# Optimization experiments

Hardware: AMD Instinct MI355X
Metric: run time of the kernel (lower is better)

Reference implementation:

```python
import jax, jax.numpy as jnp
import numpy as np

NUM_HEADS = 16


def setup_inputs() -> dict:
    key = jax.random.key(0)
    k1, k2, k3 = jax.random.split(key, 3)
    B, S, D = 2, 2048, 1024
    x = jax.random.normal(k1, (B, S, D), dtype=jnp.float32)
    # qkv_bias=False -> no bias on qkv projection; output Dense has default bias
    w_qkv = jax.random.normal(k2, (D, 3 * D), dtype=jnp.float32) * (1.0 / np.sqrt(D))
    w_out = jax.random.normal(k3, (D, D), dtype=jnp.float32) * (1.0 / np.sqrt(D))
    b_out = jnp.zeros((D,), dtype=jnp.float32)
    return {"x": x, "w_qkv": w_qkv, "w_out": w_out, "b_out": b_out}


def reference(x, w_qkv, w_out, b_out):
    B, S, D = x.shape
    H = NUM_HEADS
    Dh = D // H
    scale = 1.0 / np.sqrt(Dh).astype(np.float32)

    qkv = jnp.einsum('bsd,de->bse', x, w_qkv)           # [B,S,3D]
    q, k, v = jnp.split(qkv, 3, axis=-1)
    split = lambda t: t.reshape(B, S, H, Dh).transpose(0, 2, 1, 3)  # [B,H,S,Dh]
    q, k, v = split(q), split(k), split(v)

    attn = jnp.einsum('bhid,bhjd->bhij', q, k) * scale  # [B,H,S,S]
    # mask=None -> all-ones mask combined with causal mask => causal float mask
    causal = jnp.tril(jnp.ones((S, S), dtype=jnp.float32))[None, None]
    attn = causal * attn + (1.0 - causal) * (-1e9)
    attn = jax.nn.softmax(attn, axis=-1)

    out = jnp.einsum('bhij,bhjd->bhid', attn, v)        # [B,H,S,Dh]
    out = out.transpose(0, 2, 1, 3).reshape(B, S, D)    # merge heads
    return jnp.einsum('bsd,de->bse', out, w_out) + b_out
```

## Files before the change

kernel.cpp:

```cpp
#include <hip/hip_runtime.h>

typedef unsigned short u16;
typedef __bf16 bf16x8 __attribute__((ext_vector_type(8)));
typedef unsigned short u16x8 __attribute__((ext_vector_type(8)));
typedef float f32x4 __attribute__((ext_vector_type(4)));

union Frag { u16x8 u; bf16x8 b; };

__device__ __forceinline__ u16 f2bf(float f) {
  unsigned u = __builtin_bit_cast(unsigned, f);
  u += 0x7fff + ((u >> 16) & 1);
  return (u16)(u >> 16);
}

__device__ __forceinline__ f32x4 mfma16(bf16x8 a, bf16x8 b, f32x4 c) {
  return __builtin_amdgcn_mfma_f32_16x16x32_bf16(a, b, c, 0, 0, 0);
}

typedef const __attribute__((address_space(1))) void* as1cv;
typedef __attribute__((address_space(3))) void* as3v;

__device__ __forceinline__ void glds16(const u16* g, u16* l) {
  __builtin_amdgcn_global_load_lds((as1cv)g, (as3v)l, 16, 0, 0);
}

__global__ __launch_bounds__(256) void castf_bf(const float* __restrict__ src,
                                                u16* __restrict__ dst, int n4) {
  int i = blockIdx.x * blockDim.x + threadIdx.x;
  int stride = gridDim.x * blockDim.x;
  for (; i < n4; i += stride) {
    float4 v = ((const float4*)src)[i];
    ushort4 o;
    o.x = f2bf(v.x); o.y = f2bf(v.y); o.z = f2bf(v.z); o.w = f2bf(v.w);
    ((ushort4*)dst)[i] = o;
  }
}

__global__ __launch_bounds__(256) void cast_transpose(const float* __restrict__ src,
                                                      u16* __restrict__ dst, int K, int N) {
  __shared__ float tile[32][33];
  int tn = N >> 5;
  int bk = blockIdx.x / tn, bn = blockIdx.x % tn;
  int k0 = bk << 5, n0 = bn << 5;
  int tx = threadIdx.x, ty = threadIdx.y;
#pragma unroll
  for (int i = 0; i < 4; i++)
    tile[ty + 8 * i][tx] = src[(size_t)(k0 + ty + 8 * i) * N + n0 + tx];
  __syncthreads();
#pragma unroll
  for (int i = 0; i < 4; i++)
    dst[(size_t)(n0 + ty + 8 * i) * K + k0 + tx] = f2bf(tile[tx][ty + 8 * i]);
}

template <int FP32OUT>
__global__ __launch_bounds__(256) void gemm_bt(const u16* __restrict__ A,
                                               const u16* __restrict__ BT,
                                               void* __restrict__ Cout,
                                               const float* __restrict__ bias,
                                               int N, int K, int nbc) {
  __shared__ u16 Al[128 * 32];
  __shared__ u16 Bl[128 * 32];
  int bid = blockIdx.x;
  int br = bid / nbc, bc = bid % nbc;
  int tid = threadIdx.x;
  int w = tid >> 6, l = tid & 63;
  int lg = l >> 4, lq = l & 15;
  int wr = w >> 1, wc = w & 1;

  f32x4 acc[4][4];
#pragma unroll
  for (int m = 0; m < 4; m++)
#pragma unroll
    for (int n = 0; n < 4; n++)
      acc[m][n] = (f32x4){0.f, 0.f, 0.f, 0.f};

  const u16* Ab = A + (size_t)(br * 128 + 32 * w + (l >> 2)) * K + (l & 3) * 8;
  const u16* Bb = BT + (size_t)(bc * 128 + 32 * w + (l >> 2)) * K + (l & 3) * 8;
  u16* Ald = Al + 32 * w * 32;
  u16* Bld = Bl + 32 * w * 32;

  for (int kt = 0; kt < K; kt += 32) {
    glds16(Ab + kt, Ald);
    glds16(Ab + (size_t)16 * K + kt, Ald + 16 * 32);
    glds16(Bb + kt, Bld);
    glds16(Bb + (size_t)16 * K + kt, Bld + 16 * 32);
    __syncthreads();

    Frag af[4], bf[4];
#pragma unroll
    for (int m = 0; m < 4; m++)
      af[m].u = *(const u16x8*)(Al + (64 * wr + 16 * m + lq) * 32 + lg * 8);
#pragma unroll
    for (int n = 0; n < 4; n++)
      bf[n].u = *(const u16x8*)(Bl + (64 * wc + 16 * n + lq) * 32 + lg * 8);
#pragma unroll
    for (int m = 0; m < 4; m++)
#pragma unroll
      for (int n = 0; n < 4; n++)
        acc[m][n] = mfma16(af[m].b, bf[n].b, acc[m][n]);
    __syncthreads();
  }

  int row0 = br * 128 + 64 * wr + lg * 4;
  int col0 = bc * 128 + 64 * wc + lq;
  if (FP32OUT) {
    float* C = (float*)Cout;
#pragma unroll
    for (int n = 0; n < 4; n++) {
      float bv = bias[col0 + 16 * n];
#pragma unroll
      for (int m = 0; m < 4; m++)
#pragma unroll
        for (int r = 0; r < 4; r++)
          C[(size_t)(row0 + 16 * m + r) * N + col0 + 16 * n] = acc[m][n][r] + bv;
    }
  } else {
    u16* C = (u16*)Cout;
#pragma unroll
    for (int n = 0; n < 4; n++)
#pragma unroll
      for (int m = 0; m < 4; m++)
#pragma unroll
        for (int r = 0; r < 4; r++)
          C[(size_t)(row0 + 16 * m + r) * N + col0 + 16 * n] = f2bf(acc[m][n][r]);
  }
}

__global__ __launch_bounds__(256) void build_vt(const u16* __restrict__ qkv,
                                                u16* __restrict__ vt) {
  __shared__ u16 t[64][65];
  int bid = blockIdx.x;
  int s0 = (bid & 31) * 64;
  int bh = bid >> 5;
  int b = bh >> 4, h = bh & 15;
  int tid = threadIdx.x;
  int r = tid >> 2, c4 = (tid & 3) * 16;
  const u16* srow = qkv + (size_t)(b * 2048 + s0 + r) * 3072 + 2048 + h * 64 + c4;
  u16x8 v0 = *(const u16x8*)(srow);
  u16x8 v1 = *(const u16x8*)(srow + 8);
#pragma unroll
  for (int j = 0; j < 8; j++) { t[r][c4 + j] = v0[j]; t[r][c4 + 8 + j] = v1[j]; }
  __syncthreads();
  int dh = tid >> 2, sc = (tid & 3) * 16;
  u16 outv[16];
#pragma unroll
  for (int i = 0; i < 16; ++i) {
    int e = sc + i;
    int b32 = e >> 5, e32 = e & 31;
    int k = ((e32 >> 2) & 1) * 16 + (e32 >> 3) * 4 + (e32 & 3);
    outv[i] = t[b32 * 32 + k][dh];
  }
  u16* drow = vt + ((size_t)bh * 64 + dh) * 2048 + s0 + sc;
  *(u16x8*)drow = *(u16x8*)&outv[0];
  *(u16x8*)(drow + 8) = *(u16x8*)&outv[8];
}

__global__ __launch_bounds__(256) void flash_attn(const u16* __restrict__ qkv,
                                                  const u16* __restrict__ vt,
                                                  u16* __restrict__ aout) {
  __shared__ __align__(16) u16 pool[2][8192];
  const float SCALE = 0.125f;
  int bid = blockIdx.x;
  int qb = 31 - (bid >> 5);
  int bh = bid & 31;
  int b = bh >> 4, h = bh & 15;
  int tid = threadIdx.x;
  int w = tid >> 6, l = tid & 63;
  int lg = l >> 4, lq = l & 15;
  int q0w = qb * 64 + w * 16;
  int qidx = q0w + lq;

  const size_t rs = 3072;
  Frag qf0, qf1;
  const u16* qbase = qkv + (size_t)(b * 2048 + q0w + lq) * rs + h * 64 + lg * 8;
  qf0.u = *(const u16x8*)(qbase);
  qf1.u = *(const u16x8*)(qbase + 32);

  int srw = l >> 3;
  int scol = 8 * ((l & 7) ^ srw);
  const u16* kg = qkv + (size_t)(b * 2048) * rs + 1024 + h * 64;
  const u16* vg = vt + (size_t)bh * 64 * 2048;
  int r0 = (w * 2 + 0) * 8 + srw;
  int r1 = (w * 2 + 1) * 8 + srw;

  float m = -1e38f, lam = 0.f;
  f32x4 o[4];
#pragma unroll
  for (int d = 0; d < 4; ++d) o[d] = (f32x4){0.f, 0.f, 0.f, 0.f};
  int ntiles = qb + 1;

  glds16(kg + (size_t)r0 * rs + scol, &pool[0][(w * 2 + 0) * 512]);
  glds16(kg + (size_t)r1 * rs + scol, &pool[0][(w * 2 + 1) * 512]);
  glds16(vg + (size_t)r0 * 2048 + scol, &pool[0][4096 + (w * 2 + 0) * 512]);
  glds16(vg + (size_t)r1 * 2048 + scol, &pool[0][4096 + (w * 2 + 1) * 512]);
  __syncthreads();

  int swz = (lq & 7) << 3;
  for (int t = 0; t < ntiles; ++t) {
    int cur = t & 1;
    if (t + 1 < ntiles) {
      int kt2 = (t + 1) * 64;
      u16* nb = &pool[cur ^ 1][0];
      glds16(kg + (size_t)(kt2 + r0) * rs + scol, nb + (w * 2 + 0) * 512);
      glds16(kg + (size_t)(kt2 + r1) * rs + scol, nb + (w * 2 + 1) * 512);
      glds16(vg + (size_t)r0 * 2048 + kt2 + scol, nb + 4096 + (w * 2 + 0) * 512);
      glds16(vg + (size_t)r1 * 2048 + kt2 + scol, nb + 4096 + (w * 2 + 1) * 512);
    }
    int kt = t * 64;
    const u16* Kl = &pool[cur][0];
    const u16* Vl = &pool[cur][4096];

    f32x4 s[4];
#pragma unroll
    for (int sub = 0; sub < 4; ++sub) {
      int row = sub * 16 + lq;
      Frag k0, k1;
      k0.u = *(const u16x8*)(Kl + row * 64 + ((lg * 8) ^ swz));
      k1.u = *(const u16x8*)(Kl + row * 64 + ((32 + lg * 8) ^ swz));
      f32x4 z = {0.f, 0.f, 0.f, 0.f};
      s[sub] = mfma16(k0.b, qf0.b, z);
      s[sub] = mfma16(k1.b, qf1.b, s[sub]);
    }

    float tm = -1e38f;
    float sv[4][4];
    if (t == qb) {
#pragma unroll
      for (int sub = 0; sub < 4; ++sub)
#pragma unroll
        for (int r = 0; r < 4; ++r) {
          int key = kt + sub * 16 + lg * 4 + r;
          float v = s[sub][r] * SCALE;
          if (key > qidx) v = -1e30f;
          sv[sub][r] = v;
          tm = fmaxf(tm, v);
        }
    } else {
#pragma unroll
      for (int sub = 0; sub < 4; ++sub)
#pragma unroll
        for (int r = 0; r < 4; ++r) {
          float v = s[sub][r] * SCALE;
          sv[sub][r] = v;
          tm = fmaxf(tm, v);
        }
    }
    tm = fmaxf(tm, __shfl_xor(tm, 16));
    tm = fmaxf(tm, __shfl_xor(tm, 32));
    float mn = fmaxf(m, tm);
    float alpha = __expf(m - mn);
    float psum = 0.f;
    unsigned pp[4][2];
#pragma unroll
    for (int sub = 0; sub < 4; ++sub) {
#pragma unroll
      for (int tt = 0; tt < 2; ++tt) {
        float p0 = __expf(sv[sub][2 * tt] - mn);
        float p1 = __expf(sv[sub][2 * tt + 1] - mn);
        psum += p0 + p1;
        pp[sub][tt] = (unsigned)f2bf(p0) | ((unsigned)f2bf(p1) << 16);
      }
    }
    psum += __shfl_xor(psum, 16);
    psum += __shfl_xor(psum, 32);
    lam = lam * alpha + psum;
    m = mn;
#pragma unroll
    for (int d = 0; d < 4; ++d)
#pragma unroll
      for (int r = 0; r < 4; ++r) o[d][r] *= alpha;

#pragma unroll
    for (int hf = 0; hf < 2; ++hf) {
      union { unsigned w4[4]; u16x8 u; bf16x8 bv; } pf;
      pf.w4[0] = pp[2 * hf][0];
      pf.w4[1] = pp[2 * hf][1];
      pf.w4[2] = pp[2 * hf + 1][0];
      pf.w4[3] = pp[2 * hf + 1][1];
#pragma unroll
      for (int d = 0; d < 4; ++d) {
        int row = d * 16 + lq;
        Frag vf;
        vf.u = *(const u16x8*)(Vl + row * 64 + ((hf * 32 + lg * 8) ^ swz));
        o[d] = mfma16(vf.b, pf.bv, o[d]);
      }
    }
    __syncthreads();
  }

  float inv = 1.0f / lam;
  u16* Ost = &pool[0][0] + w * (16 * 72);
#pragma unroll
  for (int d = 0; d < 4; ++d)
#pragma unroll
    for (int r = 0; r < 4; ++r)
      Ost[lq * 72 + d * 16 + lg * 4 + r] = f2bf(o[d][r] * inv);
  int q = l >> 2, c16 = (l & 3) * 16;
  u16x8 t0, t1;
#pragma unroll
  for (int j = 0; j < 8; j++) { t0[j] = Ost[q * 72 + c16 + j]; t1[j] = Ost[q * 72 + c16 + 8 + j]; }
  u16* orow = aout + (size_t)(b * 2048 + qb * 64 + w * 16 + q) * 1024 + h * 64 + c16;
  *(u16x8*)orow = t0;
  *(u16x8*)(orow + 8) = t1;
}

extern "C" void kernel_launch(void* const* d_in, const int* in_sizes, int n_in,
                              void* d_out, int out_size, void* d_ws, size_t ws_size,
                              hipStream_t stream) {
  const float* x    = (const float*)d_in[0];
  const float* wqkv = (const float*)d_in[1];
  const float* wout = (const float*)d_in[2];
  const float* bout = (const float*)d_in[3];
  float* out = (float*)d_out;

  char* ws = (char*)d_ws;
  u16* xb    = (u16*)(ws);
  u16* wqkvT = (u16*)(ws + 8388608);
  u16* woutT = (u16*)(ws + 14680064);
  u16* qkvb  = (u16*)(ws + 16777216);
  u16* vtb   = (u16*)(ws + 41943040);
  u16* aoutb = (u16*)(ws + 50331648);

  castf_bf<<<1024, 256, 0, stream>>>(x, xb, (4096 * 1024) / 4);
  cast_transpose<<<(1024 / 32) * (3072 / 32), dim3(32, 8), 0, stream>>>(wqkv, wqkvT, 1024, 3072);
  cast_transpose<<<(1024 / 32) * (1024 / 32), dim3(32, 8), 0, stream>>>(wout, woutT, 1024, 1024);

  gemm_bt<0><<<(4096 / 128) * (3072 / 128), 256, 0, stream>>>(xb, wqkvT, qkvb, nullptr,
                                                              3072, 1024, 3072 / 128);
  build_vt<<<1024, 256, 0, stream>>>(qkvb, vtb);
  flash_attn<<<2 * 16 * (2048 / 64), 256, 0, stream>>>(qkvb, vtb, aoutb);

  gemm_bt<1><<<(4096 / 128) * (1024 / 128), 256, 0, stream>>>(aoutb, woutT, out, bout,
                                                              1024, 1024, 1024 / 128);
}
```

Baseline: 127.3 us.

## Use exp2 softmax with lazy max rescaling and MFMA priority hints in flash attention

Folds the 1/sqrt(d) scale and log2(e) into a single FMA and replaces __expf with the raw v_exp_f32 instruction. The running max and output rescale are updated only when some lane's new max exceeds the old one by more than 8 in log2 units, which skips most rescale multiplies. It also builds the P fragments directly as bf16 and wraps the MFMA sections in s_setprio hints. The lazy rescale lets probabilities grow up to 2^8 before renormalising, which affects bf16 rounding of P, and the hardware conversion may round differently from the old manual f2bf.

```diff
diff --git a/kernel.cpp b/kernel.cpp
--- a/kernel.cpp
+++ b/kernel.cpp
@@ -15,6 +15,12 @@
 
 __device__ __forceinline__ f32x4 mfma16(bf16x8 a, bf16x8 b, f32x4 c) {
   return __builtin_amdgcn_mfma_f32_16x16x32_bf16(a, b, c, 0, 0, 0);
+}
+
+__device__ __forceinline__ float exp2_raw(float x) {
+  float r;
+  asm("v_exp_f32 %0, %1" : "=v"(r) : "v"(x));
+  return r;
 }
 
 typedef const __attribute__((address_space(1))) void* as1cv;
@@ -159,58 +165,57 @@
                                                   const u16* __restrict__ vt,
                                                   u16* __restrict__ aout) {
   __shared__ __align__(16) u16 pool[2][8192];
-  const float SCALE = 0.125f;
+  const float SL2E = 0.18033688011112043f;
   int bid = blockIdx.x;
+  int bh = bid & 31;
   int qb = 31 - (bid >> 5);
-  int bh = bid & 31;
   int b = bh >> 4, h = bh & 15;
   int tid = threadIdx.x;
   int w = tid >> 6, l = tid & 63;
   int lg = l >> 4, lq = l & 15;
   int q0w = qb * 64 + w * 16;
   int qidx = q0w + lq;
+  int ntiles = qb + 1;
 
   const size_t rs = 3072;
-  Frag qf0, qf1;
-  const u16* qbase = qkv + (size_t)(b * 2048 + q0w + lq) * rs + h * 64 + lg * 8;
-  qf0.u = *(const u16x8*)(qbase);
-  qf1.u = *(const u16x8*)(qbase + 32);
-
   int srw = l >> 3;
   int scol = 8 * ((l & 7) ^ srw);
   const u16* kg = qkv + (size_t)(b * 2048) * rs + 1024 + h * 64;
   const u16* vg = vt + (size_t)bh * 64 * 2048;
   int r0 = (w * 2 + 0) * 8 + srw;
   int r1 = (w * 2 + 1) * 8 + srw;
+  int swz = (lq & 7) << 3;
+
+  Frag qf0, qf1;
+  const u16* qbase = qkv + (size_t)(b * 2048 + q0w + lq) * rs + h * 64 + lg * 8;
+  qf0.u = *(const u16x8*)(qbase);
+  qf1.u = *(const u16x8*)(qbase + 32);
 
   float m = -1e38f, lam = 0.f;
   f32x4 o[4];
 #pragma unroll
   for (int d = 0; d < 4; ++d) o[d] = (f32x4){0.f, 0.f, 0.f, 0.f};
-  int ntiles = qb + 1;
-
-  glds16(kg + (size_t)r0 * rs + scol, &pool[0][(w * 2 + 0) * 512]);
-  glds16(kg + (size_t)r1 * rs + scol, &pool[0][(w * 2 + 1) * 512]);
-  glds16(vg + (size_t)r0 * 2048 + scol, &pool[0][4096 + (w * 2 + 0) * 512]);
-  glds16(vg + (size_t)r1 * 2048 + scol, &pool[0][4096 + (w * 2 + 1) * 512]);
+
+  auto stage = [&](int tile, int buf) {
+    int kt2 = tile * 64;
+    u16* nb = &pool[buf][0];
+    glds16(kg + (size_t)(kt2 + r0) * rs + scol, nb + (w * 2 + 0) * 512);
+    glds16(kg + (size_t)(kt2 + r1) * rs + scol, nb + (w * 2 + 1) * 512);
+    glds16(vg + (size_t)r0 * 2048 + kt2 + scol, nb + 4096 + (w * 2 + 0) * 512);
+    glds16(vg + (size_t)r1 * 2048 + kt2 + scol, nb + 4096 + (w * 2 + 1) * 512);
+  };
+
+  stage(0, 0);
   __syncthreads();
 
-  int swz = (lq & 7) << 3;
   for (int t = 0; t < ntiles; ++t) {
-    int cur = t & 1;
-    if (t + 1 < ntiles) {
-      int kt2 = (t + 1) * 64;
-      u16* nb = &pool[cur ^ 1][0];
-      glds16(kg + (size_t)(kt2 + r0) * rs + scol, nb + (w * 2 + 0) * 512);
-      glds16(kg + (size_t)(kt2 + r1) * rs + scol, nb + (w * 2 + 1) * 512);
-      glds16(vg + (size_t)r0 * 2048 + kt2 + scol, nb + 4096 + (w * 2 + 0) * 512);
-      glds16(vg + (size_t)r1 * 2048 + kt2 + scol, nb + 4096 + (w * 2 + 1) * 512);
-    }
+    if (t + 1 < ntiles) stage(t + 1, (t + 1) & 1);
+    const u16* Kl = &pool[t & 1][0];
+    const u16* Vl = &pool[t & 1][4096];
     int kt = t * 64;
-    const u16* Kl = &pool[cur][0];
-    const u16* Vl = &pool[cur][4096];
 
     f32x4 s[4];
+    __builtin_amdgcn_s_setprio(1);
 #pragma unroll
     for (int sub = 0; sub < 4; ++sub) {
       int row = sub * 16 + lq;
@@ -221,70 +226,67 @@
       s[sub] = mfma16(k0.b, qf0.b, z);
       s[sub] = mfma16(k1.b, qf1.b, s[sub]);
     }
-
-    float tm = -1e38f;
-    float sv[4][4];
+    __builtin_amdgcn_s_setprio(0);
+
+    float tm_raw = -1e30f;
     if (t == qb) {
 #pragma unroll
       for (int sub = 0; sub < 4; ++sub)
 #pragma unroll
         for (int r = 0; r < 4; ++r) {
           int key = kt + sub * 16 + lg * 4 + r;
-          float v = s[sub][r] * SCALE;
-          if (key > qidx) v = -1e30f;
-          sv[sub][r] = v;
-          tm = fmaxf(tm, v);
+          if (key > qidx) s[sub][r] = -1e30f;
+          tm_raw = fmaxf(tm_raw, s[sub][r]);
         }
     } else {
 #pragma unroll
       for (int sub = 0; sub < 4; ++sub)
 #pragma unroll
-        for (int r = 0; r < 4; ++r) {
-          float v = s[sub][r] * SCALE;
-          sv[sub][r] = v;
-          tm = fmaxf(tm, v);
-        }
-    }
-    tm = fmaxf(tm, __shfl_xor(tm, 16));
-    tm = fmaxf(tm, __shfl_xor(tm, 32));
-    float mn = fmaxf(m, tm);
-    float alpha = __expf(m - mn);
+        for (int r = 0; r < 4; ++r)
+          tm_raw = fmaxf(tm_raw, s[sub][r]);
+    }
+    tm_raw = fmaxf(tm_raw, __shfl_xor(tm_raw, 16));
+    tm_raw = fmaxf(tm_raw, __shfl_xor(tm_raw, 32));
+    float tm = tm_raw * SL2E;
+
+    if (!__all(tm <= m + 8.0f)) {
+      float mn = fmaxf(m, tm);
+      float alpha = exp2_raw(m - mn);
+      lam *= alpha;
+#pragma unroll
+      for (int d = 0; d < 4; ++d)
+#pragma unroll
+        for (int r = 0; r < 4; ++r) o[d][r] *= alpha;
+      m = mn;
+    }
+
     float psum = 0.f;
-    unsigned pp[4][2];
-#pragma unroll
-    for (int sub = 0; sub < 4; ++sub) {
-#pragma unroll
-      for (int tt = 0; tt < 2; ++tt) {
-        float p0 = __expf(sv[sub][2 * tt] - mn);
-        float p1 = __expf(sv[sub][2 * tt + 1] - mn);
+    Frag pf[2];
+#pragma unroll
+    for (int hf = 0; hf < 2; ++hf)
+#pragma unroll
+      for (int r = 0; r < 4; ++r) {
+        float p0 = exp2_raw(fmaf(s[2 * hf][r], SL2E, -m));
+        float p1 = exp2_raw(fmaf(s[2 * hf + 1][r], SL2E, -m));
         psum += p0 + p1;
-        pp[sub][tt] = (unsigned)f2bf(p0) | ((unsigned)f2bf(p1) << 16);
+        pf[hf].b[r] = (__bf16)p0;
+        pf[hf].b[4 + r] = (__bf16)p1;
       }
-    }
     psum += __shfl_xor(psum, 16);
     psum += __shfl_xor(psum, 32);
-    lam = lam * alpha + psum;
-    m = mn;
-#pragma unroll
-    for (int d = 0; d < 4; ++d)
-#pragma unroll
-      for (int r = 0; r < 4; ++r) o[d][r] *= alpha;
-
-#pragma unroll
-    for (int hf = 0; hf < 2; ++hf) {
-      union { unsigned w4[4]; u16x8 u; bf16x8 bv; } pf;
-      pf.w4[0] = pp[2 * hf][0];
-      pf.w4[1] = pp[2 * hf][1];
-      pf.w4[2] = pp[2 * hf + 1][0];
-      pf.w4[3] = pp[2 * hf + 1][1];
-#pragma unroll
-      for (int d = 0; d < 4; ++d) {
-        int row = d * 16 + lq;
-        Frag vf;
-        vf.u = *(const u16x8*)(Vl + row * 64 + ((hf * 32 + lg * 8) ^ swz));
-        o[d] = mfma16(vf.b, pf.bv, o[d]);
-      }
-    }
+    lam += psum;
+
+    __builtin_amdgcn_s_setprio(1);
+#pragma unroll
+    for (int d = 0; d < 4; ++d) {
+      int row = d * 16 + lq;
+      Frag vf0, vf1;
+      vf0.u = *(const u16x8*)(Vl + row * 64 + ((lg * 8) ^ swz));
+      vf1.u = *(const u16x8*)(Vl + row * 64 + ((32 + lg * 8) ^ swz));
+      o[d] = mfma16(vf0.b, pf[0].b, o[d]);
+      o[d] = mfma16(vf1.b, pf[1].b, o[d]);
+    }
+    __builtin_amdgcn_s_setprio(0);
     __syncthreads();
   }
 
@@ -328,7 +330,7 @@
   gemm_bt<0><<<(4096 / 128) * (3072 / 128), 256, 0, stream>>>(xb, wqkvT, qkvb, nullptr,
                                                               3072, 1024, 3072 / 128);
   build_vt<<<1024, 256, 0, stream>>>(qkvb, vtb);
-  flash_attn<<<2 * 16 * (2048 / 64), 256, 0, stream>>>(qkvb, vtb, aoutb);
+  flash_attn<<<1024, 256, 0, stream>>>(qkvb, vtb, aoutb);
 
   gemm_bt<1><<<(4096 / 128) * (1024 / 128), 256, 0, stream>>>(aoutb, woutT, out, bout,
                                                               1024, 1024, 1024 / 128);
```

After: 123.5 us. -3.0%, faster.
